# Performance work log

Measured on AMD Instinct MI355X. Metric: run time of the kernel, lower is better.

Reference implementation:

```python
import jax, jax.numpy as jnp
import numpy as np

SEQ_LEN, BATCH, DIM = 128, 128, 1024

def setup_inputs() -> dict:
    key = jax.random.key(0)
    k1, k2, k3, k4 = jax.random.split(key, 4)
    scale = 1.0 / np.sqrt(DIM)
    return {
        "x": jax.random.normal(k1, (SEQ_LEN, BATCH, DIM), dtype=jnp.float32),
        "h0": jax.random.normal(k2, (BATCH, DIM), dtype=jnp.float32),
        "Wx": jax.random.normal(k3, (DIM, DIM), dtype=jnp.float32) * scale,
        "Wh": jax.random.normal(k4, (DIM, DIM), dtype=jnp.float32) * scale,
        "b": jnp.zeros((DIM,), dtype=jnp.float32),
    }

def reference(x, h0, Wx, Wh, b):
    # Vanilla tanh RNN cell scanned over seq_len (dropout is identity at keep_prob=1).
    # Precompute the input projection for all timesteps in one big GEMM.
    xp = jnp.einsum('sbi,ij->sbj', x, Wx) + b  # [S, B, H]
    def step(h, xp_t):
        h_new = jnp.tanh(xp_t + h @ Wh)
        return h_new, h_new
    _, hs = jax.lax.scan(step, h0, xp)
    return hs  # [seq_len, batch, hidden]: stacked hidden states
```

## Files before the change

kernel.cpp:

```cpp
#include <hip/hip_runtime.h>
#include <math.h>


#define DIM 1024
#define BATCH 128
#define SEQ 128
#define BD (BATCH * DIM)
#define NBLK 128
#define GRP 16
#define HSTR 1032
#define FLAGSTR 16
#define XNB 256
#define HXGRP 16384

typedef __attribute__((ext_vector_type(8))) short bf16x8;
typedef __attribute__((ext_vector_type(4))) float f32x4;

static __device__ __forceinline__ unsigned short f2bf_rne(float f) {
    unsigned u = __builtin_bit_cast(unsigned, f);
    unsigned r = (u + 0x7FFFu + ((u >> 16) & 1u)) >> 16;
    return (unsigned short)r;
}
static __device__ __forceinline__ float bf2f(unsigned short h) {
    return __builtin_bit_cast(float, ((unsigned)h) << 16);
}

static __device__ __forceinline__ void split_pair(
    unsigned long long v, unsigned& hp, unsigned& lp)
{
    const unsigned u0 = (unsigned)v;
    const unsigned u1 = (unsigned)(v >> 32);
    const float f0 = __builtin_bit_cast(float, u0);
    const float f1 = __builtin_bit_cast(float, u1);
    hp = (u0 >> 16) | (u1 & 0xFFFF0000u);
    const float r0 = f0 - __builtin_bit_cast(float, u0 & 0xFFFF0000u);
    const float r1 = f1 - __builtin_bit_cast(float, u1 & 0xFFFF0000u);
    lp = (unsigned)f2bf_rne(r0) | ((unsigned)f2bf_rne(r1) << 16);
}

__global__ __launch_bounds__(512) void xp_pers(
    const float* __restrict__ x,
    const float* __restrict__ Wx,
    const float* __restrict__ bias,
    float* __restrict__ out)
{
    __shared__ unsigned short hHi[16 * HSTR];
    __shared__ unsigned short hLo[16 * HSTR];
    __shared__ f32x4 redS[256];

    const int tid = threadIdx.x;
    const int bid = blockIdx.x;
    const int g   = bid & 15;
    const int ct  = bid >> 4;
    const int tg  = g >> 3;
    const int bt  = g & 7;
    const int B0  = bt * 16;
    const int Cb  = ct * 64;
    const int NT  = SEQ / 2;

    const int w = tid >> 6;
    const int l = tid & 63;
    const int n = l & 15;
    const int q = l >> 4;
    const int cb = Cb + (w >> 1) * 16;
    const int K0 = (w & 1) * 512;

    bf16x8 Bhi[16], Blo[16];
    #pragma unroll
    for (int s = 0; s < 16; ++s) {
        bf16x8 hi, lo;
        #pragma unroll
        for (int j = 0; j < 8; ++j) {
            const int k = K0 + 32 * s + q * 8 + j;
            const float wv = Wx[(size_t)k * DIM + cb + n];
            const unsigned short h16 = f2bf_rne(wv);
            hi[j] = (short)h16;
            lo[j] = (short)f2bf_rne(wv - bf2f(h16));
        }
        Bhi[s] = hi;
        Blo[s] = lo;
    }
    const float bv = bias[cb + n];

    const int sr = tid >> 5;
    const int su = tid & 31;

    {
        const float* xT = x + (size_t)(tg * NT) * BD + (size_t)B0 * DIM;
        const unsigned long long* srow =
            (const unsigned long long*)(xT + (size_t)sr * DIM);
        unsigned short* dh = &hHi[sr * HSTR];
        unsigned short* dl = &hLo[sr * HSTR];
        #pragma unroll
        for (int i = 0; i < 16; ++i) {
            unsigned hp, lp;
            split_pair(srow[su + 32 * i], hp, lp);
            *(unsigned*)(dh + 2 * (su + 32 * i)) = hp;
            *(unsigned*)(dl + 2 * (su + 32 * i)) = lp;
        }
    }

    for (int tt = 0; tt < NT; ++tt) {
        const int t = tg * NT + tt;
        float* outT = out + (size_t)t * BD;

        unsigned long long xr[16];
        if (tt + 1 < NT) {
            const float* xN = x + (size_t)(t + 1) * BD + (size_t)B0 * DIM;
            const unsigned long long* srow =
                (const unsigned long long*)(xN + (size_t)sr * DIM);
            #pragma unroll
            for (int i = 0; i < 16; ++i) xr[i] = srow[su + 32 * i];
        }

        __syncthreads();

        f32x4 acc = {0.f, 0.f, 0.f, 0.f};
        {
            const unsigned short* rh = &hHi[(l & 15) * HSTR + K0];
            const unsigned short* rl = &hLo[(l & 15) * HSTR + K0];
            #pragma unroll
            for (int s = 0; s < 16; ++s) {
                const bf16x8 ah = *(const bf16x8*)(rh + 32 * s + 8 * q);
                const bf16x8 al = *(const bf16x8*)(rl + 32 * s + 8 * q);
                acc = __builtin_amdgcn_mfma_f32_16x16x32_bf16(ah, Bhi[s], acc, 0, 0, 0);
                acc = __builtin_amdgcn_mfma_f32_16x16x32_bf16(al, Bhi[s], acc, 0, 0, 0);
                acc = __builtin_amdgcn_mfma_f32_16x16x32_bf16(ah, Blo[s], acc, 0, 0, 0);
            }
        }

        if (w & 1) redS[(w >> 1) * 64 + l] = acc;
        __syncthreads();

        if (!(w & 1)) {
            const f32x4 p = redS[(w >> 1) * 64 + l];
            #pragma unroll
            for (int i = 0; i < 4; ++i)
                outT[(size_t)(B0 + q * 4 + i) * DIM + cb + n] = acc[i] + p[i] + bv;
        }

        if (tt + 1 < NT) {
            unsigned short* dh = &hHi[sr * HSTR];
            unsigned short* dl = &hLo[sr * HSTR];
            #pragma unroll
            for (int i = 0; i < 16; ++i) {
                unsigned hp, lp;
                split_pair(xr[i], hp, lp);
                *(unsigned*)(dh + 2 * (su + 32 * i)) = hp;
                *(unsigned*)(dl + 2 * (su + 32 * i)) = lp;
            }
        }
    }
}

__global__ __launch_bounds__(512) void rnn_scan(
    const float* __restrict__ h0,
    const float* __restrict__ Wh,
    float* out,
    unsigned* flags,
    unsigned short* hX)
{
    __shared__ unsigned short hS[16 * HSTR];
    __shared__ f32x4 redS[256];

    const int tid = threadIdx.x;
    const int p   = blockIdx.x;
    const int bt  = p & 7;
    const int ct  = p >> 3;
    const int lbid = bt * 16 + ct;
    const int B0  = bt * 16;
    const int Cb  = ct * 64;

    const int w = tid >> 6;
    const int l = tid & 63;
    const int n = l & 15;
    const int q = l >> 4;
    const int cb = Cb + (w >> 1) * 16;
    const int K0 = (w & 1) * 512;

    bf16x8 Bhi[16], Blo[16];
    #pragma unroll
    for (int s = 0; s < 16; ++s) {
        bf16x8 hi, lo;
        #pragma unroll
        for (int j = 0; j < 8; ++j) {
            const int k = K0 + 32 * s + q * 8 + j;
            const float wv = Wh[(size_t)k * DIM + cb + n];
            const unsigned short h16 = f2bf_rne(wv);
            hi[j] = (short)h16;
            lo[j] = (short)f2bf_rne(wv - bf2f(h16));
        }
        Bhi[s] = hi;
        Blo[s] = lo;
    }

    const int sr = tid >> 5;
    const int su = tid & 31;
    const int qq = tid & 3;
    const int c0 = (tid >> 2) & 127;

    for (int t = 0; t < SEQ; ++t) {
        float* outT = out + (size_t)t * BD;

        float xpv[4];
        if (!(w & 1)) {
            #pragma unroll
            for (int i = 0; i < 4; ++i)
                xpv[i] = __builtin_nontemporal_load(
                    &outT[(size_t)(B0 + q * 4 + i) * DIM + cb + n]);
        }

        if (t == 0) {
            const float* hsrc = h0 + (size_t)B0 * DIM;
            const unsigned long long* srow =
                (const unsigned long long*)(hsrc + (size_t)sr * DIM);
            unsigned short* drow = &hS[sr * HSTR];
            #pragma unroll
            for (int i = 0; i < 16; ++i) {
                const unsigned long long v = srow[su + 32 * i];
                const float f0 = __builtin_bit_cast(float, (unsigned)(v & 0xFFFFFFFFull));
                const float f1 = __builtin_bit_cast(float, (unsigned)(v >> 32));
                const unsigned pk =
                    (unsigned)f2bf_rne(f0) | ((unsigned)f2bf_rne(f1) << 16);
                *(unsigned*)(drow + 2 * (su + 32 * i)) = pk;
            }
        } else {
            const unsigned short* gX = hX + (size_t)((t - 1) & 1) * (8 * HXGRP)
                                          + (size_t)bt * HXGRP;
            #pragma unroll
            for (int half = 0; half < 2; ++half) {
                const int cp = c0 + half * 128;
                unsigned long long L[4];
                #pragma unroll
                for (int cc = 0; cc < 4; ++cc)
                    L[cc] = __hip_atomic_load(
                        (const unsigned long long*)(gX + (size_t)(4 * cp + cc) * 16 + qq * 4),
                        __ATOMIC_RELAXED, __HIP_MEMORY_SCOPE_AGENT);
                #pragma unroll
                for (int i = 0; i < 2; ++i) {
                    const unsigned a0 = (unsigned)(L[0] >> (32 * i));
                    const unsigned a1 = (unsigned)(L[1] >> (32 * i));
                    const unsigned a2 = (unsigned)(L[2] >> (32 * i));
                    const unsigned a3 = (unsigned)(L[3] >> (32 * i));
                    const unsigned r0w0 = (a0 & 0xFFFFu) | (a1 << 16);
                    const unsigned r0w1 = (a2 & 0xFFFFu) | (a3 << 16);
                    const unsigned r1w0 = (a0 >> 16) | (a1 & 0xFFFF0000u);
                    const unsigned r1w1 = (a2 >> 16) | (a3 & 0xFFFF0000u);
                    *(unsigned long long*)&hS[(4 * qq + 2 * i) * HSTR + 4 * cp] =
                        (unsigned long long)r0w0 | ((unsigned long long)r0w1 << 32);
                    *(unsigned long long*)&hS[(4 * qq + 2 * i + 1) * HSTR + 4 * cp] =
                        (unsigned long long)r1w0 | ((unsigned long long)r1w1 << 32);
                }
            }
        }

        __syncthreads();

        f32x4 acc = {0.f, 0.f, 0.f, 0.f};
        {
            const unsigned short* hrow = &hS[(l & 15) * HSTR + K0];
            #pragma unroll
            for (int s = 0; s < 16; ++s) {
                const bf16x8 a = *(const bf16x8*)(hrow + 32 * s + 8 * q);
                acc = __builtin_amdgcn_mfma_f32_16x16x32_bf16(a, Bhi[s], acc, 0, 0, 0);
                acc = __builtin_amdgcn_mfma_f32_16x16x32_bf16(a, Blo[s], acc, 0, 0, 0);
            }
        }

        if (w & 1) redS[(w >> 1) * 64 + l] = acc;
        __syncthreads();

        if (!(w & 1)) {
            const f32x4 pp = redS[(w >> 1) * 64 + l];
            const float v0 = tanhf(acc[0] + pp[0] + xpv[0]);
            const float v1 = tanhf(acc[1] + pp[1] + xpv[1]);
            const float v2 = tanhf(acc[2] + pp[2] + xpv[2]);
            const float v3 = tanhf(acc[3] + pp[3] + xpv[3]);

            const unsigned p0 = (unsigned)f2bf_rne(v0) | ((unsigned)f2bf_rne(v1) << 16);
            const unsigned p1 = (unsigned)f2bf_rne(v2) | ((unsigned)f2bf_rne(v3) << 16);
            unsigned short* gW = hX + (size_t)(t & 1) * (8 * HXGRP) + (size_t)bt * HXGRP;
            __hip_atomic_store(
                (unsigned long long*)(gW + (size_t)(cb + n) * 16 + q * 4),
                (unsigned long long)p0 | ((unsigned long long)p1 << 32),
                __ATOMIC_RELAXED, __HIP_MEMORY_SCOPE_AGENT);

            if (t < SEQ - 1) {
                asm volatile("s_waitcnt vmcnt(0)" ::: "memory");
                if (l == 0)
                    __hip_atomic_fetch_add(&flags[lbid * FLAGSTR], 1u,
                                           __ATOMIC_RELAXED, __HIP_MEMORY_SCOPE_AGENT);
            }

            __builtin_nontemporal_store(v0, &outT[(size_t)(B0 + q * 4 + 0) * DIM + cb + n]);
            __builtin_nontemporal_store(v1, &outT[(size_t)(B0 + q * 4 + 1) * DIM + cb + n]);
            __builtin_nontemporal_store(v2, &outT[(size_t)(B0 + q * 4 + 2) * DIM + cb + n]);
            __builtin_nontemporal_store(v3, &outT[(size_t)(B0 + q * 4 + 3) * DIM + cb + n]);
        }

        if (t < SEQ - 1) {
            if (tid < GRP) {
                const unsigned need = 4u * (unsigned)(t + 1);
                const unsigned* slot = &flags[(bt * GRP + tid) * FLAGSTR];
                while (__hip_atomic_load(slot, __ATOMIC_RELAXED,
                                         __HIP_MEMORY_SCOPE_AGENT) < need)
                    __builtin_amdgcn_s_sleep(1);
            }
            __syncthreads();
        }
    }
}

extern "C" void kernel_launch(void* const* d_in, const int* in_sizes, int n_in,
                              void* d_out, int out_size, void* d_ws, size_t ws_size,
                              hipStream_t stream) {
    const float* x  = (const float*)d_in[0];
    const float* h0 = (const float*)d_in[1];
    const float* Wx = (const float*)d_in[2];
    const float* Wh = (const float*)d_in[3];
    const float* b  = (const float*)d_in[4];
    float* out = (float*)d_out;
    unsigned* flags = (unsigned*)d_ws;
    unsigned short* hX = (unsigned short*)((char*)d_ws + 8192);

    hipMemsetAsync(d_ws, 0, NBLK * FLAGSTR * sizeof(unsigned), stream);

    xp_pers<<<dim3(XNB), dim3(512), 0, stream>>>(x, Wx, b, out);

    rnn_scan<<<dim3(NBLK), dim3(512), 0, stream>>>(h0, Wh, out, flags, hX);
}
```

Before: 871.0 us.

## Fuse input projection into persistent RNN scan kernel

Removes the separate xp_pers kernel and computes x_t·Wx inside each scan step, keeping both Wx and Wh split into bf16 hi/lo register fragments. The next timestep's x is prefetched and split into shared memory while the block waits on the inter-block flag barrier, so the projection work overlaps the synchronisation. The flag protocol also changes from per-wave atomic increments to a single store of the step index after a block barrier. This avoids writing xp to out and reading it back, at the cost of extra MFMAs on the serial critical path, double the register footprint for weights, and more shared memory.

Result: slower. 1.554 ms (+78.4%).

```diff
diff --git a/kernel.cpp b/kernel.cpp
--- a/kernel.cpp
+++ b/kernel.cpp
@@ -10,7 +10,6 @@
 #define GRP 16
 #define HSTR 1032
 #define FLAGSTR 16
-#define XNB 256
 #define HXGRP 16384
 
 typedef __attribute__((ext_vector_type(8))) short bf16x8;
@@ -38,129 +37,19 @@
     lp = (unsigned)f2bf_rne(r0) | ((unsigned)f2bf_rne(r1) << 16);
 }
 
-__global__ __launch_bounds__(512) void xp_pers(
+__global__ __launch_bounds__(512) void rnn_fused(
     const float* __restrict__ x,
+    const float* __restrict__ h0,
     const float* __restrict__ Wx,
+    const float* __restrict__ Wh,
     const float* __restrict__ bias,
-    float* __restrict__ out)
-{
-    __shared__ unsigned short hHi[16 * HSTR];
-    __shared__ unsigned short hLo[16 * HSTR];
-    __shared__ f32x4 redS[256];
-
-    const int tid = threadIdx.x;
-    const int bid = blockIdx.x;
-    const int g   = bid & 15;
-    const int ct  = bid >> 4;
-    const int tg  = g >> 3;
-    const int bt  = g & 7;
-    const int B0  = bt * 16;
-    const int Cb  = ct * 64;
-    const int NT  = SEQ / 2;
-
-    const int w = tid >> 6;
-    const int l = tid & 63;
-    const int n = l & 15;
-    const int q = l >> 4;
-    const int cb = Cb + (w >> 1) * 16;
-    const int K0 = (w & 1) * 512;
-
-    bf16x8 Bhi[16], Blo[16];
-    #pragma unroll
-    for (int s = 0; s < 16; ++s) {
-        bf16x8 hi, lo;
-        #pragma unroll
-        for (int j = 0; j < 8; ++j) {
-            const int k = K0 + 32 * s + q * 8 + j;
-            const float wv = Wx[(size_t)k * DIM + cb + n];
-            const unsigned short h16 = f2bf_rne(wv);
-            hi[j] = (short)h16;
-            lo[j] = (short)f2bf_rne(wv - bf2f(h16));
-        }
-        Bhi[s] = hi;
-        Blo[s] = lo;
-    }
-    const float bv = bias[cb + n];
-
-    const int sr = tid >> 5;
-    const int su = tid & 31;
-
-    {
-        const float* xT = x + (size_t)(tg * NT) * BD + (size_t)B0 * DIM;
-        const unsigned long long* srow =
-            (const unsigned long long*)(xT + (size_t)sr * DIM);
-        unsigned short* dh = &hHi[sr * HSTR];
-        unsigned short* dl = &hLo[sr * HSTR];
-        #pragma unroll
-        for (int i = 0; i < 16; ++i) {
-            unsigned hp, lp;
-            split_pair(srow[su + 32 * i], hp, lp);
-            *(unsigned*)(dh + 2 * (su + 32 * i)) = hp;
-            *(unsigned*)(dl + 2 * (su + 32 * i)) = lp;
-        }
-    }
-
-    for (int tt = 0; tt < NT; ++tt) {
-        const int t = tg * NT + tt;
-        float* outT = out + (size_t)t * BD;
-
-        unsigned long long xr[16];
-        if (tt + 1 < NT) {
-            const float* xN = x + (size_t)(t + 1) * BD + (size_t)B0 * DIM;
-            const unsigned long long* srow =
-                (const unsigned long long*)(xN + (size_t)sr * DIM);
-            #pragma unroll
-            for (int i = 0; i < 16; ++i) xr[i] = srow[su + 32 * i];
-        }
-
-        __syncthreads();
-
-        f32x4 acc = {0.f, 0.f, 0.f, 0.f};
-        {
-            const unsigned short* rh = &hHi[(l & 15) * HSTR + K0];
-            const unsigned short* rl = &hLo[(l & 15) * HSTR + K0];
-            #pragma unroll
-            for (int s = 0; s < 16; ++s) {
-                const bf16x8 ah = *(const bf16x8*)(rh + 32 * s + 8 * q);
-                const bf16x8 al = *(const bf16x8*)(rl + 32 * s + 8 * q);
-                acc = __builtin_amdgcn_mfma_f32_16x16x32_bf16(ah, Bhi[s], acc, 0, 0, 0);
-                acc = __builtin_amdgcn_mfma_f32_16x16x32_bf16(al, Bhi[s], acc, 0, 0, 0);
-                acc = __builtin_amdgcn_mfma_f32_16x16x32_bf16(ah, Blo[s], acc, 0, 0, 0);
-            }
-        }
-
-        if (w & 1) redS[(w >> 1) * 64 + l] = acc;
-        __syncthreads();
-
-        if (!(w & 1)) {
-            const f32x4 p = redS[(w >> 1) * 64 + l];
-            #pragma unroll
-            for (int i = 0; i < 4; ++i)
-                outT[(size_t)(B0 + q * 4 + i) * DIM + cb + n] = acc[i] + p[i] + bv;
-        }
-
-        if (tt + 1 < NT) {
-            unsigned short* dh = &hHi[sr * HSTR];
-            unsigned short* dl = &hLo[sr * HSTR];
-            #pragma unroll
-            for (int i = 0; i < 16; ++i) {
-                unsigned hp, lp;
-                split_pair(xr[i], hp, lp);
-                *(unsigned*)(dh + 2 * (su + 32 * i)) = hp;
-                *(unsigned*)(dl + 2 * (su + 32 * i)) = lp;
-            }
-        }
-    }
-}
-
-__global__ __launch_bounds__(512) void rnn_scan(
-    const float* __restrict__ h0,
-    const float* __restrict__ Wh,
     float* out,
     unsigned* flags,
     unsigned short* hX)
 {
-    __shared__ unsigned short hS[16 * HSTR];
+    __shared__ unsigned short hS [16 * HSTR];
+    __shared__ unsigned short xHi[16 * HSTR];
+    __shared__ unsigned short xLo[16 * HSTR];
     __shared__ f32x4 redS[256];
 
     const int tid = threadIdx.x;
@@ -178,10 +67,10 @@
     const int cb = Cb + (w >> 1) * 16;
     const int K0 = (w & 1) * 512;
 
-    bf16x8 Bhi[16], Blo[16];
+    bf16x8 Bhi[16], Blo[16], Xhi[16], Xlo[16];
     #pragma unroll
     for (int s = 0; s < 16; ++s) {
-        bf16x8 hi, lo;
+        bf16x8 hi, lo, xh, xl;
         #pragma unroll
         for (int j = 0; j < 8; ++j) {
             const int k = K0 + 32 * s + q * 8 + j;
@@ -189,25 +78,46 @@
             const unsigned short h16 = f2bf_rne(wv);
             hi[j] = (short)h16;
             lo[j] = (short)f2bf_rne(wv - bf2f(h16));
-        }
-        Bhi[s] = hi;
-        Blo[s] = lo;
+            const float xv = Wx[(size_t)k * DIM + cb + n];
+            const unsigned short x16 = f2bf_rne(xv);
+            xh[j] = (short)x16;
+            xl[j] = (short)f2bf_rne(xv - bf2f(x16));
+        }
+        Bhi[s] = hi;  Blo[s] = lo;
+        Xhi[s] = xh;  Xlo[s] = xl;
     }
+    const float bv = bias[cb + n];
 
     const int sr = tid >> 5;
     const int su = tid & 31;
     const int qq = tid & 3;
     const int c0 = (tid >> 2) & 127;
 
+    {
+        const float* xT = x + (size_t)B0 * DIM;
+        const unsigned long long* srow =
+            (const unsigned long long*)(xT + (size_t)sr * DIM);
+        unsigned short* dh = &xHi[sr * HSTR];
+        unsigned short* dl = &xLo[sr * HSTR];
+        #pragma unroll
+        for (int i = 0; i < 16; ++i) {
+            unsigned hp, lp;
+            split_pair(srow[su + 32 * i], hp, lp);
+            *(unsigned*)(dh + 2 * (su + 32 * i)) = hp;
+            *(unsigned*)(dl + 2 * (su + 32 * i)) = lp;
+        }
+    }
+
     for (int t = 0; t < SEQ; ++t) {
         float* outT = out + (size_t)t * BD;
 
-        float xpv[4];
-        if (!(w & 1)) {
-            #pragma unroll
-            for (int i = 0; i < 4; ++i)
-                xpv[i] = __builtin_nontemporal_load(
-                    &outT[(size_t)(B0 + q * 4 + i) * DIM + cb + n]);
+        unsigned long long xr[16];
+        if (t + 1 < SEQ) {
+            const float* xN = x + (size_t)(t + 1) * BD + (size_t)B0 * DIM;
+            const unsigned long long* srow =
+                (const unsigned long long*)(xN + (size_t)sr * DIM);
+            #pragma unroll
+            for (int i = 0; i < 16; ++i) xr[i] = srow[su + 32 * i];
         }
 
         if (t == 0) {
@@ -258,25 +168,32 @@
 
         f32x4 acc = {0.f, 0.f, 0.f, 0.f};
         {
-            const unsigned short* hrow = &hS[(l & 15) * HSTR + K0];
+            const unsigned short* hrow = &hS [(l & 15) * HSTR + K0];
+            const unsigned short* xrh  = &xHi[(l & 15) * HSTR + K0];
+            const unsigned short* xrl  = &xLo[(l & 15) * HSTR + K0];
             #pragma unroll
             for (int s = 0; s < 16; ++s) {
-                const bf16x8 a = *(const bf16x8*)(hrow + 32 * s + 8 * q);
-                acc = __builtin_amdgcn_mfma_f32_16x16x32_bf16(a, Bhi[s], acc, 0, 0, 0);
-                acc = __builtin_amdgcn_mfma_f32_16x16x32_bf16(a, Blo[s], acc, 0, 0, 0);
+                const bf16x8 a  = *(const bf16x8*)(hrow + 32 * s + 8 * q);
+                const bf16x8 xh = *(const bf16x8*)(xrh  + 32 * s + 8 * q);
+                const bf16x8 xl = *(const bf16x8*)(xrl  + 32 * s + 8 * q);
+                acc = __builtin_amdgcn_mfma_f32_16x16x32_bf16(a,  Bhi[s], acc, 0, 0, 0);
+                acc = __builtin_amdgcn_mfma_f32_16x16x32_bf16(a,  Blo[s], acc, 0, 0, 0);
+                acc = __builtin_amdgcn_mfma_f32_16x16x32_bf16(xh, Xhi[s], acc, 0, 0, 0);
+                acc = __builtin_amdgcn_mfma_f32_16x16x32_bf16(xl, Xhi[s], acc, 0, 0, 0);
+                acc = __builtin_amdgcn_mfma_f32_16x16x32_bf16(xh, Xlo[s], acc, 0, 0, 0);
             }
         }
 
         if (w & 1) redS[(w >> 1) * 64 + l] = acc;
         __syncthreads();
 
+        float v0, v1, v2, v3;
         if (!(w & 1)) {
             const f32x4 pp = redS[(w >> 1) * 64 + l];
-            const float v0 = tanhf(acc[0] + pp[0] + xpv[0]);
-            const float v1 = tanhf(acc[1] + pp[1] + xpv[1]);
-            const float v2 = tanhf(acc[2] + pp[2] + xpv[2]);
-            const float v3 = tanhf(acc[3] + pp[3] + xpv[3]);
-
+            v0 = tanhf(acc[0] + pp[0] + bv);
+            v1 = tanhf(acc[1] + pp[1] + bv);
+            v2 = tanhf(acc[2] + pp[2] + bv);
+            v3 = tanhf(acc[3] + pp[3] + bv);
             const unsigned p0 = (unsigned)f2bf_rne(v0) | ((unsigned)f2bf_rne(v1) << 16);
             const unsigned p1 = (unsigned)f2bf_rne(v2) | ((unsigned)f2bf_rne(v3) << 16);
             unsigned short* gW = hX + (size_t)(t & 1) * (8 * HXGRP) + (size_t)bt * HXGRP;
@@ -284,26 +201,40 @@
                 (unsigned long long*)(gW + (size_t)(cb + n) * 16 + q * 4),
                 (unsigned long long)p0 | ((unsigned long long)p1 << 32),
                 __ATOMIC_RELAXED, __HIP_MEMORY_SCOPE_AGENT);
-
-            if (t < SEQ - 1) {
-                asm volatile("s_waitcnt vmcnt(0)" ::: "memory");
-                if (l == 0)
-                    __hip_atomic_fetch_add(&flags[lbid * FLAGSTR], 1u,
-                                           __ATOMIC_RELAXED, __HIP_MEMORY_SCOPE_AGENT);
-            }
-
+        }
+
+        if (t < SEQ - 1) {
+            asm volatile("s_waitcnt vmcnt(0)" ::: "memory");
+            __syncthreads();
+            if (tid == 0)
+                __hip_atomic_store(&flags[lbid * FLAGSTR], (unsigned)(t + 1),
+                                   __ATOMIC_RELAXED, __HIP_MEMORY_SCOPE_AGENT);
+        }
+
+        if (!(w & 1)) {
             __builtin_nontemporal_store(v0, &outT[(size_t)(B0 + q * 4 + 0) * DIM + cb + n]);
             __builtin_nontemporal_store(v1, &outT[(size_t)(B0 + q * 4 + 1) * DIM + cb + n]);
             __builtin_nontemporal_store(v2, &outT[(size_t)(B0 + q * 4 + 2) * DIM + cb + n]);
             __builtin_nontemporal_store(v3, &outT[(size_t)(B0 + q * 4 + 3) * DIM + cb + n]);
         }
 
+        if (t + 1 < SEQ) {
+            unsigned short* dh = &xHi[sr * HSTR];
+            unsigned short* dl = &xLo[sr * HSTR];
+            #pragma unroll
+            for (int i = 0; i < 16; ++i) {
+                unsigned hp, lp;
+                split_pair(xr[i], hp, lp);
+                *(unsigned*)(dh + 2 * (su + 32 * i)) = hp;
+                *(unsigned*)(dl + 2 * (su + 32 * i)) = lp;
+            }
+        }
+
         if (t < SEQ - 1) {
             if (tid < GRP) {
-                const unsigned need = 4u * (unsigned)(t + 1);
                 const unsigned* slot = &flags[(bt * GRP + tid) * FLAGSTR];
                 while (__hip_atomic_load(slot, __ATOMIC_RELAXED,
-                                         __HIP_MEMORY_SCOPE_AGENT) < need)
+                                         __HIP_MEMORY_SCOPE_AGENT) < (unsigned)(t + 1))
                     __builtin_amdgcn_s_sleep(1);
             }
             __syncthreads();
@@ -325,7 +256,6 @@
 
     hipMemsetAsync(d_ws, 0, NBLK * FLAGSTR * sizeof(unsigned), stream);
 
-    xp_pers<<<dim3(XNB), dim3(512), 0, stream>>>(x, Wx, b, out);
-
-    rnn_scan<<<dim3(NBLK), dim3(512), 0, stream>>>(h0, Wh, out, flags, hX);
-}
+    rnn_fused<<<dim3(NBLK), dim3(512), 0, stream>>>(
+        x, h0, Wx, Wh, b, out, flags, hX);
+}
```

## Replace block-wide step barrier with per-wave monotonic tags polled by consumers

Applied to the files above, without the earlier changes.

Each producing wave now publishes a monotonic step tag (a plain store of t+1) instead of bumping a per-block counter with an atomic add. Each consumer thread spins only on the two tags covering the hidden-state columns it actually loads, instead of 16 threads waiting on the whole batch group and then a __syncthreads. This removes one block-wide barrier per timestep and lets waves start loading as soon as their inputs are ready. In exchange there are more tag slots (512) and many more threads polling global memory, and correctness now relies on finer-grained relaxed ordering. The last step also skips the unused hidden-state exchange store.

New measurement: 772.3 us. 1.13x faster.

```diff
diff --git a/kernel.cpp b/kernel.cpp
--- a/kernel.cpp
+++ b/kernel.cpp
@@ -7,7 +7,6 @@
 #define SEQ 128
 #define BD (BATCH * DIM)
 #define NBLK 128
-#define GRP 16
 #define HSTR 1032
 #define FLAGSTR 16
 #define XNB 256
@@ -157,7 +156,7 @@
     const float* __restrict__ h0,
     const float* __restrict__ Wh,
     float* out,
-    unsigned* flags,
+    unsigned* tags,
     unsigned short* hX)
 {
     __shared__ unsigned short hS[16 * HSTR];
@@ -167,7 +166,6 @@
     const int p   = blockIdx.x;
     const int bt  = p & 7;
     const int ct  = p >> 3;
-    const int lbid = bt * 16 + ct;
     const int B0  = bt * 16;
     const int Cb  = ct * 64;
 
@@ -199,6 +197,10 @@
     const int qq = tid & 3;
     const int c0 = (tid >> 2) & 127;
 
+    const int myslot = bt * 64 + ct * 4 + (w >> 1);
+    const unsigned* tg0 = &tags[(bt * 64 + (c0 >> 2)) * FLAGSTR];
+    const unsigned* tg1 = &tags[(bt * 64 + 32 + (c0 >> 2)) * FLAGSTR];
+
     for (int t = 0; t < SEQ; ++t) {
         float* outT = out + (size_t)t * BD;
 
@@ -225,6 +227,15 @@
                 *(unsigned*)(drow + 2 * (su + 32 * i)) = pk;
             }
         } else {
+            const unsigned need = (unsigned)t;
+            while (__hip_atomic_load(tg0, __ATOMIC_RELAXED,
+                                     __HIP_MEMORY_SCOPE_AGENT) < need)
+                __builtin_amdgcn_s_sleep(1);
+            while (__hip_atomic_load(tg1, __ATOMIC_RELAXED,
+                                     __HIP_MEMORY_SCOPE_AGENT) < need)
+                __builtin_amdgcn_s_sleep(1);
+            asm volatile("" ::: "memory");
+
             const unsigned short* gX = hX + (size_t)((t - 1) & 1) * (8 * HXGRP)
                                           + (size_t)bt * HXGRP;
             #pragma unroll
@@ -277,36 +288,25 @@
             const float v2 = tanhf(acc[2] + pp[2] + xpv[2]);
             const float v3 = tanhf(acc[3] + pp[3] + xpv[3]);
 
-            const unsigned p0 = (unsigned)f2bf_rne(v0) | ((unsigned)f2bf_rne(v1) << 16);
-            const unsigned p1 = (unsigned)f2bf_rne(v2) | ((unsigned)f2bf_rne(v3) << 16);
-            unsigned short* gW = hX + (size_t)(t & 1) * (8 * HXGRP) + (size_t)bt * HXGRP;
-            __hip_atomic_store(
-                (unsigned long long*)(gW + (size_t)(cb + n) * 16 + q * 4),
-                (unsigned long long)p0 | ((unsigned long long)p1 << 32),
-                __ATOMIC_RELAXED, __HIP_MEMORY_SCOPE_AGENT);
-
             if (t < SEQ - 1) {
+                const unsigned p0 = (unsigned)f2bf_rne(v0) | ((unsigned)f2bf_rne(v1) << 16);
+                const unsigned p1 = (unsigned)f2bf_rne(v2) | ((unsigned)f2bf_rne(v3) << 16);
+                unsigned short* gW = hX + (size_t)(t & 1) * (8 * HXGRP)
+                                        + (size_t)bt * HXGRP;
+                __hip_atomic_store(
+                    (unsigned long long*)(gW + (size_t)(cb + n) * 16 + q * 4),
+                    (unsigned long long)p0 | ((unsigned long long)p1 << 32),
+                    __ATOMIC_RELAXED, __HIP_MEMORY_SCOPE_AGENT);
                 asm volatile("s_waitcnt vmcnt(0)" ::: "memory");
                 if (l == 0)
-                    __hip_atomic_fetch_add(&flags[lbid * FLAGSTR], 1u,
-                                           __ATOMIC_RELAXED, __HIP_MEMORY_SCOPE_AGENT);
+                    __hip_atomic_store(&tags[myslot * FLAGSTR], (unsigned)(t + 1),
+                                       __ATOMIC_RELAXED, __HIP_MEMORY_SCOPE_AGENT);
             }
 
             __builtin_nontemporal_store(v0, &outT[(size_t)(B0 + q * 4 + 0) * DIM + cb + n]);
             __builtin_nontemporal_store(v1, &outT[(size_t)(B0 + q * 4 + 1) * DIM + cb + n]);
             __builtin_nontemporal_store(v2, &outT[(size_t)(B0 + q * 4 + 2) * DIM + cb + n]);
             __builtin_nontemporal_store(v3, &outT[(size_t)(B0 + q * 4 + 3) * DIM + cb + n]);
-        }
-
-        if (t < SEQ - 1) {
-            if (tid < GRP) {
-                const unsigned need = 4u * (unsigned)(t + 1);
-                const unsigned* slot = &flags[(bt * GRP + tid) * FLAGSTR];
-                while (__hip_atomic_load(slot, __ATOMIC_RELAXED,
-                                         __HIP_MEMORY_SCOPE_AGENT) < need)
-                    __builtin_amdgcn_s_sleep(1);
-            }
-            __syncthreads();
         }
     }
 }
@@ -320,12 +320,12 @@
     const float* Wh = (const float*)d_in[3];
     const float* b  = (const float*)d_in[4];
     float* out = (float*)d_out;
-    unsigned* flags = (unsigned*)d_ws;
-    unsigned short* hX = (unsigned short*)((char*)d_ws + 8192);
-
-    hipMemsetAsync(d_ws, 0, NBLK * FLAGSTR * sizeof(unsigned), stream);
+    unsigned* tags = (unsigned*)d_ws;
+    unsigned short* hX = (unsigned short*)((char*)d_ws + 32768);
+
+    hipMemsetAsync(d_ws, 0, 512 * FLAGSTR * sizeof(unsigned), stream);
 
     xp_pers<<<dim3(XNB), dim3(512), 0, stream>>>(x, Wx, b, out);
 
-    rnn_scan<<<dim3(NBLK), dim3(512), 0, stream>>>(h0, Wh, out, flags, hX);
-}
+    rnn_scan<<<dim3(NBLK), dim3(512), 0, stream>>>(h0, Wh, out, tags, hX);
+}
```
